# Kernel optimization log

Measured on AMD Instinct MI355X. Metric: run time of the kernel, lower is better.

## Reference

```python
import jax, jax.numpy as jnp
import numpy as np


def setup_inputs() -> dict:
    key = jax.random.key(0)
    k1, k2, k3, k4, k5, k6 = jax.random.split(key, 6)
    H = 1024
    B, La, Lq = 32, 512, 64
    # kaiming_uniform with a=sqrt(5) on [H,H]: bound = sqrt(6/((1+5)*H)) = 1/sqrt(H)
    bound = 1.0 / np.sqrt(H)
    return {
        "article_feature": jax.random.normal(k1, (B, La, H), dtype=jnp.float32),
        "query_op_feature": jax.random.normal(k2, (B, Lq, H), dtype=jnp.float32),
        "weight1_1": jax.random.uniform(k3, (H, H), minval=-bound, maxval=bound, dtype=jnp.float32),
        "weight1_2": jax.random.uniform(k4, (H, H), minval=-bound, maxval=bound, dtype=jnp.float32),
        "weight2_1": jax.random.uniform(k5, (H, H), minval=-bound, maxval=bound, dtype=jnp.float32),
        "weight2_2": jax.random.uniform(k6, (H, H), minval=-bound, maxval=bound, dtype=jnp.float32),
    }


def reference(article_feature, query_op_feature, weight1_1, weight1_2, weight2_1, weight2_2):
    # article_feature: [B, La, H], query_op_feature: [B, Lq, H]
    # aq_attention: softmax over Lq of (A @ W1_1) @ Q^T -> [B, La, Lq]
    aq_scores = jnp.einsum("bah,hk,bqk->baq", article_feature, weight1_1, query_op_feature)
    aq_attention = jax.nn.softmax(aq_scores, axis=2)
    # qa_attention: softmax over La of (Q @ W1_2) @ A^T -> [B, Lq, La]
    qa_scores = jnp.einsum("bqh,hk,bak->bqa", query_op_feature, weight1_2, article_feature)
    qa_attention = jax.nn.softmax(qa_scores, axis=2)
    # S_a: relu((aq_attention @ Q) @ W2_1) -> [B, La, H]
    S_a = jax.nn.relu(jnp.einsum("baq,bqh,hk->bak", aq_attention, query_op_feature, weight2_1))
    # S_q: relu((qa_attention @ A) @ W2_2) -> [B, Lq, H]
    S_q = jax.nn.relu(jnp.einsum("bqa,bah,hk->bqk", qa_attention, article_feature, weight2_2))
    S_aq = jnp.max(S_a, axis=1)  # [B, H]
    S_qa = jnp.max(S_q, axis=1)  # [B, H]
    g = jnp.float32(0.5)
    return g * S_aq + (1.0 - g) * S_qa
```

## Files before the change

kernel.cpp:

```cpp
#include <hip/hip_runtime.h>
#include <stdint.h>


using f16x8 = __attribute__((ext_vector_type(8))) _Float16;
using f32x4 = __attribute__((ext_vector_type(4))) float;
typedef const __attribute__((address_space(1))) void* gas_t;
typedef __attribute__((address_space(3))) void* las_t;

__device__ __forceinline__ unsigned short f2h(float x) {
  _Float16 h = (_Float16)x;
  return __builtin_bit_cast(unsigned short, h);
}


__global__ __launch_bounds__(256) void prep_all(
    const float* __restrict__ W11, const float* __restrict__ W12,
    const float* __restrict__ W21, const float* __restrict__ W22,
    const float* __restrict__ Qfeat,
    unsigned short* __restrict__ Wcat, unsigned short* __restrict__ W21T,
    unsigned short* __restrict__ W22T, unsigned short* __restrict__ Q_hi)
{
  int z = blockIdx.z;
  int tx = threadIdx.x, ty = threadIdx.y;
  if (z >= 4) {
    int blk = (z - 4) * 1024 + blockIdx.y * 32 + blockIdx.x;
    int i = blk * 256 + ty * 32 + tx;
    float4 v = ((const float4*)Qfeat)[i];
    ushort4 h;
    h.x = f2h(v.x); h.y = f2h(v.y); h.z = f2h(v.z); h.w = f2h(v.w);
    ((ushort4*)Q_hi)[i] = h;
    return;
  }
  __shared__ float tile[32][33];
  const float* src = z == 0 ? W11 : z == 1 ? W12 : z == 2 ? W21 : W22;
  int r0 = blockIdx.y * 32, c0 = blockIdx.x * 32;
  #pragma unroll
  for (int i = 0; i < 4; ++i) {
    int r = r0 + ty + i * 8;
    float v = src[(long)r * 1024 + c0 + tx];
    tile[ty + i * 8][tx] = v;
    if (z == 0) Wcat[(long)r * 1024 + c0 + tx] = f2h(v);
  }
  __syncthreads();
  if (z > 0) {
    #pragma unroll
    for (int i = 0; i < 4; ++i) {
      float v = tile[tx][ty + i * 8];
      long o = (long)(c0 + ty + i * 8) * 1024 + r0 + tx;
      if (z == 1)      Wcat[1048576 + o] = f2h(v);
      else if (z == 2) W21T[o] = f2h(v);
      else             W22T[o] = f2h(v);
    }
  }
}

template<int BM, int BN, int OUT, bool BF32, int NC>
__device__ __forceinline__ void gemm_body(
    char* smem, int bx, int by, int z,
    const unsigned short* __restrict__ Ah,
    const unsigned short* __restrict__ Bh, const float* __restrict__ Bf,
    float* __restrict__ Cf, unsigned short* __restrict__ Ch,
    int M, int N, int K, int ldA, int ldB, int ldC, long sA, long sB, long sC)
{
  constexpr int ACH = BM * 64, BCH = BN * 64;
  constexpr int MI = BM / 32, NI = BN / 32;
  char* As = smem;
  char* Bs = smem + NC * ACH;

  const int m0 = by * BM, n0 = bx * BN;
  const int t = threadIdx.x, lane = t & 63;
  const int wid = t >> 6, wr = wid >> 1, wc = wid & 1;

  const unsigned short* Ab = Ah + (long)z * sA;
  const unsigned short* Bb = BF32 ? nullptr : Bh + (long)z * sB;
  const float* Bfb = BF32 ? Bf + (long)z * sB : nullptr;

  f32x4 acc[MI][NI];
  #pragma unroll
  for (int i = 0; i < MI; ++i)
    #pragma unroll
    for (int j = 0; j < NI; ++j)
      acc[i][j] = f32x4{0.f, 0.f, 0.f, 0.f};

  auto stage4k = [&](char* lbuf, const unsigned short* g, int ld, int row0, int k0, int rmax) {
    int ob = t * 16;
    int e  = ob ^ (((ob >> 7) & 3) << 4);
    int m  = e >> 6, k = (e & 63) >> 1;
    int row = row0 + m; row = row < rmax ? row : rmax - 1;
    const unsigned short* gp = g + (long)row * ld + k0 + k;
    char* lp = lbuf + (t & ~63) * 16;
    __builtin_amdgcn_global_load_lds((gas_t)(const void*)gp, (las_t)(void*)lp, 16, 0, 0);
  };
  auto stageB_f32 = [&](char* lbuf, const float* g, int ld, int nb, int k0) {
    int ob = t * 16;
    int e  = ob ^ (((ob >> 7) & 3) << 4);
    int n  = e >> 6, kb = (e & 63) >> 1;
    f16x8 pk;
    #pragma unroll
    for (int j = 0; j < 8; ++j) {
      float v = g[(long)(k0 + kb + j) * ld + nb + n];
      pk[j] = (_Float16)v;
    }
    *(f16x8*)(lbuf + ob) = pk;
  };
  auto ldfrag = [&](const char* lbuf, int rr) -> f16x8 {
    int ob = rr * 64 + (lane >> 4) * 16;
    ob ^= ((ob >> 7) & 3) << 4;
    return *(const f16x8*)(lbuf + ob);
  };
  auto compute32 = [&](const char* Ac, const char* Bc) {
    f16x8 ah[MI];
    #pragma unroll
    for (int mi = 0; mi < MI; ++mi)
      ah[mi] = ldfrag(Ac, wr * (BM / 2) + mi * 16 + (lane & 15));
    #pragma unroll
    for (int ni = 0; ni < NI; ++ni) {
      f16x8 bh = ldfrag(Bc, wc * (BN / 2) + ni * 16 + (lane & 15));
      #pragma unroll
      for (int mi = 0; mi < MI; ++mi)
        acc[mi][ni] = __builtin_amdgcn_mfma_f32_16x16x32_f16(ah[mi], bh, acc[mi][ni], 0, 0, 0);
    }
  };

  for (int k0 = 0; k0 < K; k0 += 32 * NC) {
    #pragma unroll
    for (int c = 0; c < NC; ++c) {
      stage4k(As + c * ACH, Ab, ldA, m0, k0 + 32 * c, M);
      if (BM == 128) stage4k(As + c * ACH + 4096, Ab, ldA, m0 + 64, k0 + 32 * c, M);
    }
    #pragma unroll
    for (int c = 0; c < NC; ++c) {
      if (BF32) stageB_f32(Bs + c * BCH, Bfb, ldB, n0, k0 + 32 * c);
      else      stage4k(Bs + c * BCH, Bb, ldB, n0, k0 + 32 * c, N);
    }
    __syncthreads();
    #pragma unroll
    for (int c = 0; c < NC; ++c) compute32(As + c * ACH, Bs + c * BCH);
    __syncthreads();
  }

  if (OUT == 6) {
    float* red = (float*)smem;
    #pragma unroll
    for (int ni = 0; ni < NI; ++ni) {
      float pm = 0.0f;
      #pragma unroll
      for (int mi = 0; mi < MI; ++mi)
        #pragma unroll
        for (int r = 0; r < 4; ++r)
          pm = fmaxf(pm, acc[mi][ni][r]);
      int g = wr * 4 + (lane >> 4);
      int col = wc * (BN / 2) + ni * 16 + (lane & 15);
      red[g * BN + col] = pm;
    }
    __syncthreads();
    if (t < BN) {
      float pq = red[t];
      #pragma unroll
      for (int g = 1; g < 8; ++g) pq = fmaxf(pq, red[g * BN + t]);
      float pa = Bf[(long)(by * 4) * 1024 + n0 + t];
      #pragma unroll
      for (int mt = 1; mt < 4; ++mt)
        pa = fmaxf(pa, Bf[(long)(by * 4 + mt) * 1024 + n0 + t]);
      Cf[(long)by * 1024 + n0 + t] = 0.5f * pa + 0.5f * pq;
    }
    return;
  }

  #pragma unroll
  for (int mi = 0; mi < MI; ++mi) {
    #pragma unroll
    for (int r = 0; r < 4; ++r) {
      int grow = m0 + wr * (BM / 2) + mi * 16 + (lane >> 4) * 4 + r;
      #pragma unroll
      for (int ni = 0; ni < NI; ++ni) {
        int gcol = n0 + wc * (BN / 2) + ni * 16 + (lane & 15);
        float v = acc[mi][ni][r];
        if (OUT == 1) {
          int b = grow >> 6, q = grow & 63;
          long dst = (long)b * 131072 + (long)((gcol >> 10) * 64 + q) * 1024 + (gcol & 1023);
          Ch[dst] = f2h(v);
        } else if (OUT == 2) {
          if (grow < M) Ch[(long)z * sC + (long)grow * ldC + gcol] = f2h(v);
        } else if (OUT == 3) {
          long dst = (long)(grow >> 6) * 65536 + (long)gcol * 64 + (grow & 63);
          Ch[dst] = f2h(v);
        }
      }
    }
  }
}


__global__ __launch_bounds__(256) void g1_kernel(
    const unsigned short* Q_hi, const unsigned short* Wcat, const unsigned short* W21T,
    unsigned short* Pcat, unsigned short* P3T)
{
  __shared__ char smem[49152];
  int bid = blockIdx.x;
  if (bid < 512) {
    gemm_body<128, 64, 1, false, 4>(smem, bid & 31, bid >> 5, 0,
        Q_hi, Wcat, nullptr, nullptr, Pcat,
        2048, 2048, 1024, 1024, 1024, 0, 0, 0, 0);
  } else {
    int b2 = bid - 512;
    gemm_body<128, 64, 3, false, 4>(smem, b2 & 15, b2 >> 4, 0,
        Q_hi, W21T, nullptr, nullptr, P3T,
        2048, 1024, 1024, 1024, 1024, 0, 0, 0, 0);
  }
}


__global__ __launch_bounds__(512) void g2_kernel(
    const float* __restrict__ Afeat, const unsigned short* __restrict__ Pcat,
    unsigned short* __restrict__ aq, float* __restrict__ Spar)
{
  __shared__ char smem[20480];
  char* A0 = smem;
  char* A1 = smem + 2048;
  char* B0 = smem + 4096;
  char* B1 = smem + 12288;

  int orig = blockIdx.x;
  int xcd = orig & 7, idx = orig >> 3;
  int z   = xcd * 4 + (idx >> 4);
  int mt  = idx & 15;
  const int m0 = mt * 32;
  const int t = threadIdx.x, lane = t & 63;
  const int wid = t >> 6, wr = wid >> 2, wc = wid & 3;

  const float* Ab = Afeat + (long)z * 524288;
  const unsigned short* Bb = Pcat + (long)z * 131072;

  f32x4 acc[2];
  acc[0] = f32x4{0.f, 0.f, 0.f, 0.f};
  acc[1] = f32x4{0.f, 0.f, 0.f, 0.f};

  auto ldfrag = [&](const char* lbuf, int rr) -> f16x8 {
    int ob = rr * 64 + (lane >> 4) * 16;
    ob ^= ((ob >> 7) & 3) << 4;
    return *(const f16x8*)(lbuf + ob);
  };
  auto stageA = [&](int k0) {
    int half = t >> 8, tt = t & 255;
    int ob = tt * 8;
    int e  = ob ^ (((ob >> 7) & 3) << 4);
    int m  = e >> 6, ke = (e & 63) >> 1;
    float4 v = *(const float4*)(Ab + (long)(m0 + m) * 1024 + k0 + half * 32 + ke);
    ushort4 h;
    h.x = f2h(v.x); h.y = f2h(v.y); h.z = f2h(v.z); h.w = f2h(v.w);
    *(ushort4*)((half ? A1 : A0) + ob) = h;
  };
  auto stageB = [&](char* lbuf, int k0) {
    int ob = t * 16;
    int e  = ob ^ (((ob >> 7) & 3) << 4);
    int n  = e >> 6, kk = (e & 63) >> 1;
    const unsigned short* gp = Bb + (long)n * 1024 + k0 + kk;
    char* lp = lbuf + (t & ~63) * 16;
    __builtin_amdgcn_global_load_lds((gas_t)(const void*)gp, (las_t)(void*)lp, 16, 0, 0);
  };
  auto compute32 = [&](const char* Ac, const char* Bc) {
    f16x8 ah = ldfrag(Ac, wr * 16 + (lane & 15));
    #pragma unroll
    for (int ni = 0; ni < 2; ++ni) {
      f16x8 bh = ldfrag(Bc, wc * 32 + ni * 16 + (lane & 15));
      acc[ni] = __builtin_amdgcn_mfma_f32_16x16x32_f16(ah, bh, acc[ni], 0, 0, 0);
    }
  };

  for (int k0 = 0; k0 < 1024; k0 += 64) {
    stageA(k0);
    stageB(B0, k0);
    stageB(B1, k0 + 32);
    __syncthreads();
    compute32(A0, B0);
    compute32(A1, B1);
    __syncthreads();
  }

  float* red = (float*)smem;
  #pragma unroll
  for (int ni = 0; ni < 2; ++ni)
    #pragma unroll
    for (int r = 0; r < 4; ++r) {
      int lrow = wr * 16 + (lane >> 4) * 4 + r;
      int col  = wc * 32 + ni * 16 + (lane & 15);
      red[lrow * 128 + col] = acc[ni][r];
    }
  __syncthreads();

  int row = t >> 4, cg = (t & 15) * 4;
  float a0 = red[row * 128 + cg],     a1 = red[row * 128 + cg + 1];
  float a2 = red[row * 128 + cg + 2], a3 = red[row * 128 + cg + 3];
  float4 vq = *(float4*)&red[row * 128 + 64 + cg];
  float mx = fmaxf(fmaxf(a0, a1), fmaxf(a2, a3));
  #pragma unroll
  for (int off = 8; off; off >>= 1) mx = fmaxf(mx, __shfl_xor(mx, off));
  float e0 = __expf(a0 - mx), e1 = __expf(a1 - mx);
  float e2 = __expf(a2 - mx), e3 = __expf(a3 - mx);
  float s = (e0 + e1) + (e2 + e3);
  #pragma unroll
  for (int off = 8; off; off >>= 1) s += __shfl_xor(s, off);
  float inv = 1.0f / s;
  ushort4 h;
  h.x = f2h(e0 * inv); h.y = f2h(e1 * inv); h.z = f2h(e2 * inv); h.w = f2h(e3 * inv);
  long base = (long)z * 32768 + (long)(m0 + row) * 64 + cg;
  *(ushort4*)(aq + base) = h;
  *(float4*)(Spar + base) = vq;
}


__global__ __launch_bounds__(256) void softmax_cols(const float* __restrict__ Sp,
                                                    unsigned short* __restrict__ qa)
{
  int bq = blockIdx.x;
  int b = bq >> 6, q = bq & 63;
  int t = threadIdx.x;
  const float* base = Sp + (long)b * 32768 + q;
  float v0 = base[(long)t * 64];
  float v1 = base[(long)(t + 256) * 64];
  float m = fmaxf(v0, v1);
  #pragma unroll
  for (int off = 32; off; off >>= 1) m = fmaxf(m, __shfl_xor(m, off));
  __shared__ float sm[4], ss[4];
  int wid = t >> 6, lane = t & 63;
  if (lane == 0) sm[wid] = m;
  __syncthreads();
  float M = fmaxf(fmaxf(sm[0], sm[1]), fmaxf(sm[2], sm[3]));
  float e0 = __expf(v0 - M), e1 = __expf(v1 - M);
  float s = e0 + e1;
  #pragma unroll
  for (int off = 32; off; off >>= 1) s += __shfl_xor(s, off);
  if (lane == 0) ss[wid] = s;
  __syncthreads();
  float inv = 1.0f / ((ss[0] + ss[1]) + (ss[2] + ss[3]));
  qa[(long)bq * 512 + t]       = f2h(e0 * inv);
  qa[(long)bq * 512 + t + 256] = f2h(e1 * inv);
}


__global__ __launch_bounds__(256) void g3_kernel(
    const unsigned short* aq, const unsigned short* P3T, float* PmaxA,
    const unsigned short* qa, const float* Afeat, unsigned short* ctx)
{
  __shared__ char smem[16384];
  int bid = blockIdx.x;
  if (bid < 1024) {
    int bx = bid & 7, by = (bid >> 3) & 3, z = bid >> 5;
    int n0 = bx * 128, m0 = by * 128;
    const unsigned short* Aq = aq + (long)z * 32768;
    const unsigned short* Bp = P3T + (long)z * 65536;
    const int t = threadIdx.x, lane = t & 63;
    const int wid = t >> 6, wr = wid >> 1, wc = wid & 1;

    f32x4 acc[4][4];
    #pragma unroll
    for (int i = 0; i < 4; ++i)
      #pragma unroll
      for (int j = 0; j < 4; ++j)
        acc[i][j] = f32x4{0.f, 0.f, 0.f, 0.f};

    #pragma unroll
    for (int c = 0; c < 2; ++c) {
      f16x8 ah[4];
      #pragma unroll
      for (int mi = 0; mi < 4; ++mi) {
        int row = m0 + wr * 64 + mi * 16 + (lane & 15);
        ah[mi] = *(const f16x8*)(Aq + (long)row * 64 + c * 32 + (lane >> 4) * 8);
      }
      #pragma unroll
      for (int ni = 0; ni < 4; ++ni) {
        int rc = n0 + wc * 64 + ni * 16 + (lane & 15);
        f16x8 bh = *(const f16x8*)(Bp + (long)rc * 64 + c * 32 + (lane >> 4) * 8);
        #pragma unroll
        for (int mi = 0; mi < 4; ++mi)
          acc[mi][ni] = __builtin_amdgcn_mfma_f32_16x16x32_f16(ah[mi], bh, acc[mi][ni], 0, 0, 0);
      }
    }

    float* red = (float*)smem;
    #pragma unroll
    for (int ni = 0; ni < 4; ++ni) {
      float pm = 0.0f;
      #pragma unroll
      for (int mi = 0; mi < 4; ++mi)
        #pragma unroll
        for (int r = 0; r < 4; ++r)
          pm = fmaxf(pm, acc[mi][ni][r]);
      int g = wr * 4 + (lane >> 4);
      int col = wc * 64 + ni * 16 + (lane & 15);
      red[g * 128 + col] = pm;
    }
    __syncthreads();
    if (t < 128) {
      float m = red[t];
      #pragma unroll
      for (int g = 1; g < 8; ++g) m = fmaxf(m, red[g * 128 + t]);
      PmaxA[(long)(z * 4 + by) * 1024 + n0 + t] = m;
    }
  } else {
    int b2 = bid - 1024;
    gemm_body<64, 64, 2, true, 2>(smem, b2 & 15, 0, b2 >> 4,
        qa, nullptr, Afeat, nullptr, ctx,
        64, 1024, 512, 512, 1024, 1024, 32768L, 524288L, 65536L);
  }
}


__global__ __launch_bounds__(256) void g4_kernel(
    const unsigned short* ctx, const unsigned short* W22T,
    const float* PmaxA, float* out)
{
  __shared__ char smem[32768];
  gemm_body<64, 64, 6, false, 4>(smem, blockIdx.x, blockIdx.y, 0,
      ctx, W22T, PmaxA, out, nullptr,
      2048, 1024, 1024, 1024, 1024, 1024, 0, 0, 0);
}


extern "C" void kernel_launch(void* const* d_in, const int* in_sizes, int n_in,
                              void* d_out, int out_size, void* d_ws, size_t ws_size,
                              hipStream_t stream) {
  const float* Afeat = (const float*)d_in[0];
  const float* Qfeat = (const float*)d_in[1];
  const float* W11   = (const float*)d_in[2];
  const float* W12   = (const float*)d_in[3];
  const float* W21   = (const float*)d_in[4];
  const float* W22   = (const float*)d_in[5];
  float* out = (float*)d_out;

  char* w = (char*)d_ws;
  auto alloc = [&](long bytes) { char* p = w; w += bytes; return p; };
  unsigned short* Q_hi  = (unsigned short*)alloc(4194304);
  unsigned short* Wcat  = (unsigned short*)alloc(4194304);
  unsigned short* W21T  = (unsigned short*)alloc(2097152);
  unsigned short* W22T  = (unsigned short*)alloc(2097152);
  unsigned short* Pcat  = (unsigned short*)alloc(8388608);
  unsigned short* P3T   = (unsigned short*)alloc(4194304);
  float*          Spar  = (float*)alloc(4194304);
  unsigned short* aq    = (unsigned short*)alloc(2097152);
  unsigned short* qa    = (unsigned short*)alloc(2097152);
  unsigned short* ctx   = (unsigned short*)alloc(4194304);
  float*          PmaxA = (float*)alloc(524288);

  dim3 blk(256), tblk(32, 8);

  prep_all<<<dim3(32, 32, 6), tblk, 0, stream>>>(W11, W12, W21, W22, Qfeat,
                                                 Wcat, W21T, W22T, Q_hi);
  g1_kernel<<<768, blk, 0, stream>>>(Q_hi, Wcat, W21T, Pcat, P3T);
  g2_kernel<<<512, dim3(512), 0, stream>>>(Afeat, Pcat, aq, Spar);
  softmax_cols<<<2048, blk, 0, stream>>>(Spar, qa);
  g3_kernel<<<1536, blk, 0, stream>>>(aq, P3T, PmaxA, qa, Afeat, ctx);
  g4_kernel<<<dim3(16, 32), blk, 0, stream>>>(ctx, W22T, PmaxA, out);
}
```

Before: 92.94 us.

## Fuse fp32-to-fp16 conversion into GEMM staging and drop prep kernel

```diff
diff --git a/kernel.cpp b/kernel.cpp
--- a/kernel.cpp
+++ b/kernel.cpp
@@ -12,55 +12,13 @@
   return __builtin_bit_cast(unsigned short, h);
 }
 
-
-__global__ __launch_bounds__(256) void prep_all(
-    const float* __restrict__ W11, const float* __restrict__ W12,
-    const float* __restrict__ W21, const float* __restrict__ W22,
-    const float* __restrict__ Qfeat,
-    unsigned short* __restrict__ Wcat, unsigned short* __restrict__ W21T,
-    unsigned short* __restrict__ W22T, unsigned short* __restrict__ Q_hi)
-{
-  int z = blockIdx.z;
-  int tx = threadIdx.x, ty = threadIdx.y;
-  if (z >= 4) {
-    int blk = (z - 4) * 1024 + blockIdx.y * 32 + blockIdx.x;
-    int i = blk * 256 + ty * 32 + tx;
-    float4 v = ((const float4*)Qfeat)[i];
-    ushort4 h;
-    h.x = f2h(v.x); h.y = f2h(v.y); h.z = f2h(v.z); h.w = f2h(v.w);
-    ((ushort4*)Q_hi)[i] = h;
-    return;
-  }
-  __shared__ float tile[32][33];
-  const float* src = z == 0 ? W11 : z == 1 ? W12 : z == 2 ? W21 : W22;
-  int r0 = blockIdx.y * 32, c0 = blockIdx.x * 32;
-  #pragma unroll
-  for (int i = 0; i < 4; ++i) {
-    int r = r0 + ty + i * 8;
-    float v = src[(long)r * 1024 + c0 + tx];
-    tile[ty + i * 8][tx] = v;
-    if (z == 0) Wcat[(long)r * 1024 + c0 + tx] = f2h(v);
-  }
-  __syncthreads();
-  if (z > 0) {
-    #pragma unroll
-    for (int i = 0; i < 4; ++i) {
-      float v = tile[tx][ty + i * 8];
-      long o = (long)(c0 + ty + i * 8) * 1024 + r0 + tx;
-      if (z == 1)      Wcat[1048576 + o] = f2h(v);
-      else if (z == 2) W21T[o] = f2h(v);
-      else             W22T[o] = f2h(v);
-    }
-  }
-}
-
-template<int BM, int BN, int OUT, bool BF32, int NC>
+template<int BM, int BN, int OUT, int ASRC, int BSRC, int NC>
 __device__ __forceinline__ void gemm_body(
     char* smem, int bx, int by, int z,
-    const unsigned short* __restrict__ Ah,
+    const unsigned short* __restrict__ Ah, const float* __restrict__ Af,
     const unsigned short* __restrict__ Bh, const float* __restrict__ Bf,
-    float* __restrict__ Cf, unsigned short* __restrict__ Ch,
-    int M, int N, int K, int ldA, int ldB, int ldC, long sA, long sB, long sC)
+    const float* __restrict__ Paux, float* __restrict__ Cf, unsigned short* __restrict__ Ch,
+    int M, int N, int K, int ldA, int ldB, int ldC, long sA, long sB, long sC, int n0B)
 {
   constexpr int ACH = BM * 64, BCH = BN * 64;
   constexpr int MI = BM / 32, NI = BN / 32;
@@ -71,9 +29,10 @@
   const int t = threadIdx.x, lane = t & 63;
   const int wid = t >> 6, wr = wid >> 1, wc = wid & 1;
 
-  const unsigned short* Ab = Ah + (long)z * sA;
-  const unsigned short* Bb = BF32 ? nullptr : Bh + (long)z * sB;
-  const float* Bfb = BF32 ? Bf + (long)z * sB : nullptr;
+  const unsigned short* Ab16 = (ASRC == 0) ? Ah + (long)z * sA : nullptr;
+  const float*          Abf  = (ASRC == 1) ? Af + (long)z * sA : nullptr;
+  const unsigned short* Bb16 = (BSRC == 0) ? Bh + (long)z * sB : nullptr;
+  const float*          Bbf  = (BSRC != 0) ? Bf + (long)z * sB : nullptr;
 
   f32x4 acc[MI][NI];
   #pragma unroll
@@ -91,16 +50,26 @@
     char* lp = lbuf + (t & ~63) * 16;
     __builtin_amdgcn_global_load_lds((gas_t)(const void*)gp, (las_t)(void*)lp, 16, 0, 0);
   };
-  auto stageB_f32 = [&](char* lbuf, const float* g, int ld, int nb, int k0) {
+  auto stageRowF32 = [&](char* lbuf, const float* g, int ld, int row0, int k0) {
+    int ob = t * 16;
+    int e  = ob ^ (((ob >> 7) & 3) << 4);
+    int m  = e >> 6, ke = (e & 63) >> 1;
+    const float* src = g + (long)(row0 + m) * ld + k0 + ke;
+    float4 v0 = *(const float4*)src;
+    float4 v1 = *(const float4*)(src + 4);
+    f16x8 pk;
+    pk[0] = (_Float16)v0.x; pk[1] = (_Float16)v0.y; pk[2] = (_Float16)v0.z; pk[3] = (_Float16)v0.w;
+    pk[4] = (_Float16)v1.x; pk[5] = (_Float16)v1.y; pk[6] = (_Float16)v1.z; pk[7] = (_Float16)v1.w;
+    *(f16x8*)(lbuf + ob) = pk;
+  };
+  auto stageKF32 = [&](char* lbuf, const float* g, int ld, int nb, int k0) {
     int ob = t * 16;
     int e  = ob ^ (((ob >> 7) & 3) << 4);
     int n  = e >> 6, kb = (e & 63) >> 1;
     f16x8 pk;
     #pragma unroll
-    for (int j = 0; j < 8; ++j) {
-      float v = g[(long)(k0 + kb + j) * ld + nb + n];
-      pk[j] = (_Float16)v;
-    }
+    for (int j = 0; j < 8; ++j)
+      pk[j] = (_Float16)g[(long)(k0 + kb + j) * ld + nb + n];
     *(f16x8*)(lbuf + ob) = pk;
   };
   auto ldfrag = [&](const char* lbuf, int rr) -> f16x8 {
@@ -125,13 +94,23 @@
   for (int k0 = 0; k0 < K; k0 += 32 * NC) {
     #pragma unroll
     for (int c = 0; c < NC; ++c) {
-      stage4k(As + c * ACH, Ab, ldA, m0, k0 + 32 * c, M);
-      if (BM == 128) stage4k(As + c * ACH + 4096, Ab, ldA, m0 + 64, k0 + 32 * c, M);
+      int kc = k0 + 32 * c;
+      char* Ac = As + c * ACH;
+      if (ASRC == 0) {
+        stage4k(Ac, Ab16, ldA, m0, kc, M);
+        if (BM == 128) stage4k(Ac + 4096, Ab16, ldA, m0 + 64, kc, M);
+      } else {
+        stageRowF32(Ac, Abf, ldA, m0, kc);
+        if (BM == 128) stageRowF32(Ac + 4096, Abf, ldA, m0 + 64, kc);
+      }
     }
     #pragma unroll
     for (int c = 0; c < NC; ++c) {
-      if (BF32) stageB_f32(Bs + c * BCH, Bfb, ldB, n0, k0 + 32 * c);
-      else      stage4k(Bs + c * BCH, Bb, ldB, n0, k0 + 32 * c, N);
+      int kc = k0 + 32 * c;
+      char* Bc = Bs + c * BCH;
+      if (BSRC == 0)      stage4k(Bc, Bb16, ldB, n0, kc, N);
+      else if (BSRC == 1) stageRowF32(Bc, Bbf, ldB, n0B, kc);
+      else                stageKF32(Bc, Bbf, ldB, n0B, kc);
     }
     __syncthreads();
     #pragma unroll
@@ -158,10 +137,10 @@
       float pq = red[t];
       #pragma unroll
       for (int g = 1; g < 8; ++g) pq = fmaxf(pq, red[g * BN + t]);
-      float pa = Bf[(long)(by * 4) * 1024 + n0 + t];
+      float pa = Paux[(long)(by * 4) * 1024 + n0 + t];
       #pragma unroll
       for (int mt = 1; mt < 4; ++mt)
-        pa = fmaxf(pa, Bf[(long)(by * 4 + mt) * 1024 + n0 + t]);
+        pa = fmaxf(pa, Paux[(long)(by * 4 + mt) * 1024 + n0 + t]);
       Cf[(long)by * 1024 + n0 + t] = 0.5f * pa + 0.5f * pq;
     }
     return;
@@ -193,20 +172,27 @@
 
 
 __global__ __launch_bounds__(256) void g1_kernel(
-    const unsigned short* Q_hi, const unsigned short* Wcat, const unsigned short* W21T,
-    unsigned short* Pcat, unsigned short* P3T)
+    const float* __restrict__ Qf, const float* __restrict__ W11,
+    const float* __restrict__ W12, const float* __restrict__ W21,
+    unsigned short* __restrict__ Pcat, unsigned short* __restrict__ P3T)
 {
   __shared__ char smem[49152];
   int bid = blockIdx.x;
   if (bid < 512) {
-    gemm_body<128, 64, 1, false, 4>(smem, bid & 31, bid >> 5, 0,
-        Q_hi, Wcat, nullptr, nullptr, Pcat,
-        2048, 2048, 1024, 1024, 1024, 0, 0, 0, 0);
+    int bx = bid & 31, by = bid >> 5;
+    if (bx < 16)
+      gemm_body<128, 64, 1, 1, 1, 4>(smem, bx, by, 0,
+          nullptr, Qf, nullptr, W11, nullptr, nullptr, Pcat,
+          2048, 2048, 1024, 1024, 1024, 0, 0, 0, 0, bx * 64);
+    else
+      gemm_body<128, 64, 1, 1, 2, 4>(smem, bx, by, 0,
+          nullptr, Qf, nullptr, W12, nullptr, nullptr, Pcat,
+          2048, 2048, 1024, 1024, 1024, 0, 0, 0, 0, (bx - 16) * 64);
   } else {
     int b2 = bid - 512;
-    gemm_body<128, 64, 3, false, 4>(smem, b2 & 15, b2 >> 4, 0,
-        Q_hi, W21T, nullptr, nullptr, P3T,
-        2048, 1024, 1024, 1024, 1024, 0, 0, 0, 0);
+    gemm_body<128, 64, 3, 1, 2, 4>(smem, b2 & 15, b2 >> 4, 0,
+        nullptr, Qf, nullptr, W21, nullptr, nullptr, P3T,
+        2048, 1024, 1024, 1024, 1024, 0, 0, 0, 0, (b2 & 15) * 64);
   }
 }
 
@@ -400,21 +386,21 @@
     }
   } else {
     int b2 = bid - 1024;
-    gemm_body<64, 64, 2, true, 2>(smem, b2 & 15, 0, b2 >> 4,
-        qa, nullptr, Afeat, nullptr, ctx,
-        64, 1024, 512, 512, 1024, 1024, 32768L, 524288L, 65536L);
+    gemm_body<64, 64, 2, 0, 2, 2>(smem, b2 & 15, 0, b2 >> 4,
+        qa, nullptr, nullptr, Afeat, nullptr, nullptr, ctx,
+        64, 1024, 512, 512, 1024, 1024, 32768L, 524288L, 65536L, (b2 & 15) * 64);
   }
 }
 
 
 __global__ __launch_bounds__(256) void g4_kernel(
-    const unsigned short* ctx, const unsigned short* W22T,
+    const unsigned short* ctx, const float* W22,
     const float* PmaxA, float* out)
 {
   __shared__ char smem[32768];
-  gemm_body<64, 64, 6, false, 4>(smem, blockIdx.x, blockIdx.y, 0,
-      ctx, W22T, PmaxA, out, nullptr,
-      2048, 1024, 1024, 1024, 1024, 1024, 0, 0, 0);
+  gemm_body<64, 64, 6, 0, 2, 4>(smem, blockIdx.x, blockIdx.y, 0,
+      ctx, nullptr, nullptr, W22, PmaxA, out, nullptr,
+      2048, 1024, 1024, 1024, 1024, 1024, 0, 0, 0, blockIdx.x * 64);
 }
 
 
@@ -431,10 +417,6 @@
 
   char* w = (char*)d_ws;
   auto alloc = [&](long bytes) { char* p = w; w += bytes; return p; };
-  unsigned short* Q_hi  = (unsigned short*)alloc(4194304);
-  unsigned short* Wcat  = (unsigned short*)alloc(4194304);
-  unsigned short* W21T  = (unsigned short*)alloc(2097152);
-  unsigned short* W22T  = (unsigned short*)alloc(2097152);
   unsigned short* Pcat  = (unsigned short*)alloc(8388608);
   unsigned short* P3T   = (unsigned short*)alloc(4194304);
   float*          Spar  = (float*)alloc(4194304);
@@ -443,13 +425,11 @@
   unsigned short* ctx   = (unsigned short*)alloc(4194304);
   float*          PmaxA = (float*)alloc(524288);
 
-  dim3 blk(256), tblk(32, 8);
-
-  prep_all<<<dim3(32, 32, 6), tblk, 0, stream>>>(W11, W12, W21, W22, Qfeat,
-                                                 Wcat, W21T, W22T, Q_hi);
-  g1_kernel<<<768, blk, 0, stream>>>(Q_hi, Wcat, W21T, Pcat, P3T);
+  dim3 blk(256);
+
+  g1_kernel<<<768, blk, 0, stream>>>(Qfeat, W11, W12, W21, Pcat, P3T);
   g2_kernel<<<512, dim3(512), 0, stream>>>(Afeat, Pcat, aq, Spar);
   softmax_cols<<<2048, blk, 0, stream>>>(Spar, qa);
   g3_kernel<<<1536, blk, 0, stream>>>(aq, P3T, PmaxA, qa, Afeat, ctx);
-  g4_kernel<<<dim3(16, 32), blk, 0, stream>>>(ctx, W22T, PmaxA, out);
-}
+  g4_kernel<<<dim3(16, 32), blk, 0, stream>>>(ctx, W22, PmaxA, out);
+}
```

After: 124.6 us. 1.34x slower.
